# Kernel tuning notes

Hardware: AMD Instinct MI355X
Metric: run time of the kernel (lower is better)

Reference implementation:

```python
import jax, jax.numpy as jnp
import numpy as np

B, C, D, H, W = 2, 16, 64, 64, 64
HD, WD = 128, 128            # X-ray detector size
P = 3                        # offset_points
SPACING = (1.0, 1.0, 1.0)
SDR = 200.0
DEL = 2.0
BN_EPS = 1e-5


def _xray_coords(D, H, W, Hd, Wd, spacing, sdr, del_size):
    """Replicates _get_initial_xray geometry; pure constants -> numpy. Returns [D,H,W,2] float32."""
    theta, phi, gamma = np.pi, 0.0, np.pi / 2
    Rz = np.array([[np.cos(theta), -np.sin(theta), 0.0], [np.sin(theta), np.cos(theta), 0.0], [0.0, 0.0, 1.0]])
    Ry = np.array([[np.cos(phi), 0.0, np.sin(phi)], [0.0, 1.0, 0.0], [-np.sin(phi), 0.0, np.cos(phi)]])
    Rx = np.array([[1.0, 0.0, 0.0], [0.0, np.cos(gamma), -np.sin(gamma)], [0.0, np.sin(gamma), np.cos(gamma)]])
    R = sdr * (Rz @ Ry @ Rx)
    trans = np.array([D, H, W]) * np.array(spacing) / 2.0
    source = R[:, 0] + trans           # [3]
    center = -R[:, 0] + trans          # [3]
    Rn = R / np.linalg.norm(R, axis=-1, keepdims=True)   # row-normalize (torch normalize dim=-1)
    u, v = Rn[:, 1], Rn[:, 2]
    basis = np.stack([u, v])           # [2,3]
    h_off = 1.0 if Hd % 2 else 0.5
    w_off = 1.0 if Wd % 2 else 0.5
    t = (np.arange(-Hd // 2, Hd // 2) + h_off) * del_size
    s = (np.arange(-Wd // 2, Wd // 2) + w_off) * del_size
    coefs = np.stack(np.meshgrid(t, s, indexing='ij'), -1).reshape(-1, 2)   # cartesian_prod(t,s)
    target = coefs @ basis + center    # [Hd*Wd, 3]
    tz = np.arange(D) * spacing[2]
    tx = np.arange(H) * spacing[0]
    ty = np.arange(W) * spacing[1]
    pz, px_, py_ = np.meshgrid(tz, tx, ty, indexing='ij')
    p_n = np.stack([pz.ravel(), px_.ravel(), py_.ravel()], 1)   # [D*H*W, 3]
    wgt = (center[0] - source[0]) / (p_n[:, 0] - source[0])
    X = wgt[:, None] * (p_n - source) + source
    tmin = target.min(0)
    tmax = target.max(0)
    X = np.clip(X, tmin, tmax)
    delta = np.array([del_size, del_size]) @ basis              # [3]; component 0 is 0 and dropped
    Xc = (X[:, 1:] - tmin[1:]) / delta[1:]
    return Xc.reshape(D, H, W, 2).astype(np.float32)


def _conv3d(x, w, b):
    y = jax.lax.conv_general_dilated(x, w, (1, 1, 1), ((1, 1), (1, 1), (1, 1)),
                                     dimension_numbers=('NCDHW', 'OIDHW', 'NCDHW'))
    return y + b[None, :, None, None, None]


def _corner_weights(py, px, y0, y1, x0, x1):
    y0f, y1f = y0.astype(py.dtype), y1.astype(py.dtype)
    x0f, x1f = x0.astype(px.dtype), x1.astype(px.dtype)
    g_lt = (1 + (y0f - py)) * (1 + (x0f - px))
    g_rb = (1 - (y1f - py)) * (1 - (x1f - px))
    g_rt = (1 + (y0f - py)) * (1 - (x1f - px))
    g_lb = (1 - (y1f - py)) * (1 + (x0f - px))
    return g_lt, g_rb, g_rt, g_lb


def _corners(py, px, Ht, Wt):
    fy, fx = jnp.floor(py), jnp.floor(px)
    y0 = jnp.clip(fy, 0, Ht - 1).astype(jnp.int32)
    y1 = jnp.clip(fy + 1, 0, Ht - 1).astype(jnp.int32)
    x0 = jnp.clip(fx, 0, Wt - 1).astype(jnp.int32)
    x1 = jnp.clip(fx + 1, 0, Wt - 1).astype(jnp.int32)
    return y0, y1, x0, x1


def _bilerp_single(p, x):
    # p: [D,H,W,2] batch-independent coords; x: [B,C,Ht,Wt]
    Bx, Cx, Ht, Wt = x.shape
    py, px = p[..., 0], p[..., 1]
    y0, y1, x0, x1 = _corners(py, px, Ht, Wt)
    glt, grb, grt, glb = _corner_weights(py, px, y0, y1, x0, x1)
    xf = x.reshape(Bx, Cx, Ht * Wt)
    gat = lambda yy, xx: jnp.take(xf, yy * Wt + xx, axis=2)   # [B,C,D,H,W]
    return glt * gat(y0, x0) + grb * gat(y1, x1) + grt * gat(y0, x1) + glb * gat(y1, x0)


def _bilerp_multi(py, px, x):
    # py, px: [B,D,H,W,P]; x: [B,C,Ht,Wt] (padded X-ray)
    Bx, Cx, Ht, Wt = x.shape
    y0, y1, x0, x1 = _corners(py, px, Ht, Wt)
    glt, grb, grt, glb = _corner_weights(py, px, y0, y1, x0, x1)
    xf = x.reshape(Bx, Cx, Ht * Wt)

    def gat(yy, xx):
        idx = yy * Wt + xx                                    # [B,D,H,W,P]
        g = jax.vmap(lambda xb, ib: jnp.take(xb, ib, axis=1))(xf, idx.reshape(Bx, -1))
        return g.reshape(Bx, Cx, *idx.shape[1:])              # [B,C,D,H,W,P]

    e = lambda g: g[:, None]                                  # add channel dim
    return e(glt) * gat(y0, x0) + e(grb) * gat(y1, x1) + e(grt) * gat(y0, x1) + e(glb) * gat(y1, x0)


def _forward(CT, Xray, pW, pb, mW, mb, w1, b1, w2, b2, bn_gamma, bn_beta, bn_mean, bn_var):
    Bc, Cc, Dc, Hc, Wc = CT.shape
    Hd, Wd = Xray.shape[2], Xray.shape[3]
    Pp = mW.shape[0]
    Xrc = jnp.asarray(_xray_coords(Dc, Hc, Wc, Hd, Wd, SPACING, SDR, DEL))   # [D,H,W,2]
    xi = _bilerp_single(Xrc, Xray)                        # [B,C,D,H,W]
    CT_mix = jnp.concatenate([CT, xi], axis=1)            # [B,2C,D,H,W]
    Xp = jnp.pad(Xray, ((0, 0), (0, 0), (1, 1), (1, 1)))  # ZeroPad2d(1)
    offset = _conv3d(CT_mix, pW, pb)                      # [B,2P,D,H,W]
    m = jax.nn.softmax(_conv3d(CT_mix, mW, mb), axis=1)   # [B,P,D,H,W]
    oc = jnp.transpose(offset, (0, 2, 3, 4, 1))           # [B,D,H,W,2P]
    py = jnp.clip(oc[..., :Pp] + Xrc[..., :1] + 1.0, 0, Hd + 1)
    px = jnp.clip(oc[..., Pp:] + Xrc[..., 1:] + 1.0, 0, Wd + 1)
    p_coor = jnp.concatenate([py, px], axis=-1)
    Xoff = _bilerp_multi(py, px, Xp)                      # [B,C,D,H,W,P]
    mm = jnp.transpose(m, (0, 2, 3, 4, 1))[:, None]       # [B,1,D,H,W,P]
    Xsum = jnp.sum(Xoff * mm, axis=-1)                    # [B,C,D,H,W]
    h = _conv3d(jnp.concatenate([CT, Xsum], axis=1), w1, b1)
    sh = (1, -1, 1, 1, 1)
    h = (h - bn_mean.reshape(sh)) * jax.lax.rsqrt(bn_var.reshape(sh) + BN_EPS) * bn_gamma.reshape(sh) + bn_beta.reshape(sh)
    h = jnp.where(h >= 0, h, 0.2 * h)                     # LeakyReLU(0.2)
    return _conv3d(h, w2, b2), p_coor


def setup_inputs() -> dict:
    key = jax.random.key(0)
    ks = jax.random.split(key, 16)
    return {
        'CT': jax.random.normal(ks[0], (B, C, D, H, W), jnp.float32),
        'Xray': jax.random.normal(ks[1], (B, C, HD, WD), jnp.float32),
        'pW': jax.random.normal(ks[2], (2 * P, 2 * C, 3, 3, 3), jnp.float32) * 0.02,
        'pb': jax.random.normal(ks[3], (2 * P,), jnp.float32) * 0.01,
        'mW': jax.random.normal(ks[4], (P, 2 * C, 3, 3, 3), jnp.float32) * 0.02,
        'mb': jax.random.normal(ks[5], (P,), jnp.float32) * 0.01,
        'w1': jax.random.normal(ks[6], (C, 2 * C, 3, 3, 3), jnp.float32) * 0.02,
        'b1': jax.random.normal(ks[7], (C,), jnp.float32) * 0.01,
        'w2': jax.random.normal(ks[8], (C, C, 3, 3, 3), jnp.float32) * 0.02,
        'b2': jax.random.normal(ks[9], (C,), jnp.float32) * 0.01,
        'bn_gamma': 1.0 + 0.1 * jax.random.normal(ks[10], (C,), jnp.float32),
        'bn_beta': 0.1 * jax.random.normal(ks[11], (C,), jnp.float32),
        'bn_mean': 0.1 * jax.random.normal(ks[12], (C,), jnp.float32),
        'bn_var': jax.random.uniform(ks[13], (C,), jnp.float32, 0.5, 1.5),
    }


def reference(CT, Xray, pW, pb, mW, mb, w1, b1, w2, b2, bn_gamma, bn_beta, bn_mean, bn_var):
    return _forward(CT, Xray, pW, pb, mW, mb, w1, b1, w2, b2, bn_gamma, bn_beta, bn_mean, bn_var)
```

## Files before the change

### kernel.cpp

```cpp
#include <hip/hip_runtime.h>
#include <hip/hip_bf16.h>
#include <math.h>

constexpr int Dd = 64, Hh = 64, Ww = 64;
constexpr int HD = 128, WD = 128;
constexpr int DHW = Dd * Hh * Ww;
constexpr int HW = Hh * Ww;
constexpr int PD = 66;
constexpr int PS3 = PD * PD * PD;
constexpr int XT_S = 128 * 128;
constexpr int XP_S = 130 * 130;

using short8 = __attribute__((ext_vector_type(8))) short;
using f32x4  = __attribute__((ext_vector_type(4))) float;

struct Geom {
    double s0, s1, s2;
    double c0ms0;
    double tmin1, tmax1, tmin2, tmax2;
    double d1, d2;
};

__device__ __forceinline__ void xray_coord(const Geom g, int z, int x, int y,
                                           float& py, float& px) {
    double wgt = g.c0ms0 / ((double)z - g.s0);
    double X1 = wgt * ((double)x - g.s1) + g.s1;
    X1 = fmin(fmax(X1, g.tmin1), g.tmax1);
    double X2 = wgt * ((double)y - g.s2) + g.s2;
    X2 = fmin(fmax(X2, g.tmin2), g.tmax2);
    py = (float)((X1 - g.tmin1) / g.d1);
    px = (float)((X2 - g.tmin2) / g.d2);
}

__device__ __forceinline__ float bf2f(unsigned short u) {
    union { unsigned int i; float f; } v;
    v.i = ((unsigned int)u) << 16;
    return v.f;
}
__device__ __forceinline__ unsigned short f2bf(float f) {
    __hip_bfloat16 h = __float2bfloat16(f);
    return *reinterpret_cast<unsigned short*>(&h);
}

template <int CIN, int NK>
__global__ __launch_bounds__(256) void k_wprep(const float* __restrict__ w6,
                                               const float* __restrict__ w3,
                                               unsigned short* __restrict__ wB) {
    int i = blockIdx.x * 256 + threadIdx.x;
    if (i >= NK * 64 * 8) return;
    int s = i >> 9, l = (i >> 3) & 63, j = i & 7;
    int n = l & 15, q = l >> 4;
    int k = s * 32 + q * 8 + j;
    int tap = k / CIN, ci = k % CIN;
    float v = 0.f;
    if (tap < 27) {
        if (w3 == nullptr) {
            v = w6[(n * CIN + ci) * 27 + tap];
        } else {
            if (n < 6) v = w6[(n * CIN + ci) * 27 + tap];
            else if (n < 9) v = w3[((n - 6) * CIN + ci) * 27 + tap];
        }
    }
    wB[i] = f2bf(v);
}

__global__ void k_bias9(const float* __restrict__ pb, const float* __restrict__ mb,
                        float* __restrict__ b9) {
    int i = threadIdx.x;
    if (i < 16) b9[i] = (i < 6) ? pb[i] : ((i < 9) ? mb[i - 6] : 0.f);
}

__global__ __launch_bounds__(256) void k_xrayT(const float* __restrict__ X,
                                               unsigned short* __restrict__ XT) {
    int i = blockIdx.x * 256 + threadIdx.x;
    if (i >= 2 * XT_S) return;
    int b = i / XT_S, sp = i % XT_S;
    const float* src = X + (size_t)b * 16 * XT_S + sp;
    unsigned short* o = XT + (size_t)i * 16;
#pragma unroll
    for (int c = 0; c < 16; ++c) o[c] = f2bf(src[(size_t)c * XT_S]);
}

__global__ __launch_bounds__(256) void k_xpT(const float* __restrict__ X,
                                             unsigned short* __restrict__ XP) {
    int i = blockIdx.x * 256 + threadIdx.x;
    if (i >= 2 * XP_S) return;
    int b = i / XP_S, rc = i % XP_S;
    int r = rc / 130, c = rc % 130;
    unsigned short o[16];
    if (r >= 1 && r <= 128 && c >= 1 && c <= 128) {
        const float* src = X + (size_t)b * 16 * XT_S + (r - 1) * 128 + (c - 1);
#pragma unroll
        for (int ch = 0; ch < 16; ++ch) o[ch] = f2bf(src[(size_t)ch * XT_S]);
    } else {
#pragma unroll
        for (int ch = 0; ch < 16; ++ch) o[ch] = 0;
    }
    uint4* dst = (uint4*)(XP + (size_t)i * 16);
    uint4* s4 = (uint4*)o;
    dst[0] = s4[0]; dst[1] = s4[1];
}

__global__ __launch_bounds__(256) void k_prep_nin(const float* __restrict__ CT,
                                                  const unsigned short* __restrict__ XT,
                                                  unsigned short* __restrict__ nin,
                                                  Geom g) {
    int vox = blockIdx.x * 256 + threadIdx.x;
    int b = blockIdx.y;
    int z = vox >> 12, x = (vox >> 6) & 63, y = vox & 63;
    unsigned short outv[32];
    const float* ct = CT + (size_t)b * 16 * DHW + vox;
#pragma unroll
    for (int c = 0; c < 16; ++c) outv[c] = f2bf(ct[(size_t)c * DHW]);
    float py, px;
    xray_coord(g, z, x, y, py, px);
    float fy = floorf(py), fx = floorf(px);
    int y0 = (int)fminf(fmaxf(fy, 0.f), 127.f);
    int y1 = (int)fminf(fmaxf(fy + 1.f, 0.f), 127.f);
    int x0 = (int)fminf(fmaxf(fx, 0.f), 127.f);
    int x1 = (int)fminf(fmaxf(fx + 1.f, 0.f), 127.f);
    float y0f = (float)y0, y1f = (float)y1, x0f = (float)x0, x1f = (float)x1;
    float glt = (1.f + (y0f - py)) * (1.f + (x0f - px));
    float grb = (1.f - (y1f - py)) * (1.f - (x1f - px));
    float grt = (1.f + (y0f - py)) * (1.f - (x1f - px));
    float glb = (1.f - (y1f - py)) * (1.f + (x0f - px));
    const unsigned short* base = XT + (size_t)b * XT_S * 16;
    const unsigned short* p00 = base + (size_t)(y0 * 128 + x0) * 16;
    const unsigned short* p11 = base + (size_t)(y1 * 128 + x1) * 16;
    const unsigned short* p01 = base + (size_t)(y0 * 128 + x1) * 16;
    const unsigned short* p10 = base + (size_t)(y1 * 128 + x0) * 16;
#pragma unroll
    for (int c = 0; c < 16; ++c) {
        float v = glt * bf2f(p00[c]) + grb * bf2f(p11[c]) +
                  grt * bf2f(p01[c]) + glb * bf2f(p10[c]);
        outv[16 + c] = f2bf(v);
    }
    size_t pp = (((size_t)(z + 1)) * PD + (x + 1)) * PD + (y + 1);
    uint4* dst = (uint4*)(nin + ((size_t)b * PS3 + pp) * 32);
    uint4* s4 = (uint4*)outv;
    dst[0] = s4[0]; dst[1] = s4[1]; dst[2] = s4[2]; dst[3] = s4[3];
}

template <int CIN, int NK, int MODE>
__global__ __launch_bounds__(256) void k_conv_mfma(
    const unsigned short* __restrict__ IN, const unsigned short* __restrict__ wB,
    const float* __restrict__ bias,
    const float* __restrict__ bng, const float* __restrict__ bnb,
    const float* __restrict__ bnm, const float* __restrict__ bnv,
    float* __restrict__ outF, unsigned short* __restrict__ outH) {
    constexpr int NSLOT = CIN / 8;
    constexpr int SSH = (NSLOT == 4) ? 2 : 1;
    constexpr int NCHUNK = NSLOT * 648;
    __shared__ unsigned short lds[NSLOT * 648 * 8];

    int tid = threadIdx.x;
    int bid = blockIdx.x;
    int zt = bid & 15, xt = (bid >> 4) & 15, yt = bid >> 8;
    int b = blockIdx.y;

    const unsigned short* gsrc = IN + (size_t)b * PS3 * CIN;
    for (int d = tid; d < NCHUNK; d += 256) {
        int slot = d & (NSLOT - 1);
        int sp = d >> SSH;
        int zz = sp / 108;
        int rem = sp - zz * 108;
        int xx = rem / 18, yy = rem - xx * 18;
        size_t gp = (((size_t)(zt * 4 + zz)) * PD + (xt * 4 + xx)) * PD + (yt * 16 + yy);
        uint4 v = *(const uint4*)(gsrc + gp * CIN + slot * 8);
        *(uint4*)&lds[(size_t)(slot * 648 + sp) * 8] = v;
    }

    int lane = tid & 63;
    short8 bw[NK];
    {
        const short8* wsrc = (const short8*)wB;
#pragma unroll
        for (int s = 0; s < NK; ++s) bw[s] = wsrc[s * 64 + lane];
    }
    int col = lane & 15, q = lane >> 4;
    float bcol = bias[col];
    float bsc = 1.f, bsh = 0.f;
    if (MODE == 1) {
        float sc = bng[col] * rsqrtf(bnv[col] + 1e-5f);
        bsc = sc;
        bsh = bnb[col] - bnm[col] * sc;
    }
    __syncthreads();

    int w = tid >> 6;
    for (int vx = 0; vx < 4; ++vx) {
        f32x4 acc = {0.f, 0.f, 0.f, 0.f};
#pragma unroll
        for (int s = 0; s < NK; ++s) {
            int tap = (s * 32 + q * 8) / CIN;
            if (CIN == 16) tap = min(tap, 26);
            int slot = q & (NSLOT - 1);
            int dz = tap / 9;
            int trem = tap - dz * 9;
            int dx = trem / 3, dy = trem - dx * 3;
            int addr = ((slot * 648) + (w + dz) * 108 + (vx + dx) * 18 + col + dy) * 8;
            short8 a = *(const short8*)&lds[addr];
            acc = __builtin_amdgcn_mfma_f32_16x16x32_bf16(a, bw[s], acc, 0, 0, 0);
        }
        int z = zt * 4 + w, x = xt * 4 + vx;
        int yb = yt * 16 + q * 4;
        if (MODE == 0) {
            int vox = z * HW + x * 64 + yb;
            float* o = outF + ((size_t)b * DHW + vox) * 16 + col;
#pragma unroll
            for (int r = 0; r < 4; ++r) o[(size_t)r * 16] = acc[r] + bcol;
        } else if (MODE == 1) {
            size_t pp = (((size_t)(z + 1)) * PD + (x + 1)) * PD + (yb + 1);
            unsigned short* o = outH + ((size_t)b * PS3 + pp) * 16 + col;
#pragma unroll
            for (int r = 0; r < 4; ++r) {
                float v = acc[r] + bcol;
                v = v * bsc + bsh;
                v = (v >= 0.f) ? v : 0.2f * v;
                o[(size_t)r * 16] = f2bf(v);
            }
        } else {
            int vox = z * HW + x * 64 + yb;
            float* o = outF + ((size_t)b * 16 + col) * DHW + vox;
#pragma unroll
            for (int r = 0; r < 4; ++r) o[r] = acc[r] + bcol;
        }
    }
}

__global__ __launch_bounds__(256) void k_deform2(const float* __restrict__ offm,
                                                 const unsigned short* __restrict__ XP,
                                                 unsigned short* __restrict__ nin,
                                                 float* __restrict__ pcoor, Geom g) {
    int idx = blockIdx.x * 256 + threadIdx.x;
    int b = idx >> 18;
    int vox = idx & (DHW - 1);
    int z = vox >> 12, x = (vox >> 6) & 63, y = vox & 63;
    float bpy, bpx;
    xray_coord(g, z, x, y, bpy, bpx);
    const float* ob = offm + ((size_t)b * DHW + vox) * 16;
    float off[6];
#pragma unroll
    for (int k = 0; k < 6; ++k) off[k] = ob[k];
    float mv0 = ob[6], mv1 = ob[7], mv2 = ob[8];
    float mx = fmaxf(mv0, fmaxf(mv1, mv2));
    float e0 = __expf(mv0 - mx), e1 = __expf(mv1 - mx), e2 = __expf(mv2 - mx);
    float inv = 1.f / (e0 + e1 + e2);
    float ms[3] = {e0 * inv, e1 * inv, e2 * inv};

    float pys[3], pxs[3];
#pragma unroll
    for (int p = 0; p < 3; ++p) {
        pys[p] = fminf(fmaxf(off[p] + bpy + 1.f, 0.f), 129.f);
        pxs[p] = fminf(fmaxf(off[3 + p] + bpx + 1.f, 0.f), 129.f);
    }
    float* pc = pcoor + (size_t)idx * 6;
    pc[0] = pys[0]; pc[1] = pys[1]; pc[2] = pys[2];
    pc[3] = pxs[0]; pc[4] = pxs[1]; pc[5] = pxs[2];

    float acc[16];
#pragma unroll
    for (int c = 0; c < 16; ++c) acc[c] = 0.f;
    const unsigned short* xpb = XP + (size_t)b * XP_S * 16;
#pragma unroll
    for (int p = 0; p < 3; ++p) {
        float py = pys[p], px = pxs[p];
        float fy = floorf(py), fx = floorf(px);
        int y0 = (int)fminf(fmaxf(fy, 0.f), 129.f);
        int y1 = (int)fminf(fmaxf(fy + 1.f, 0.f), 129.f);
        int x0 = (int)fminf(fmaxf(fx, 0.f), 129.f);
        int x1 = (int)fminf(fmaxf(fx + 1.f, 0.f), 129.f);
        float y0f = (float)y0, y1f = (float)y1, x0f = (float)x0, x1f = (float)x1;
        float glt = (1.f + (y0f - py)) * (1.f + (x0f - px));
        float grb = (1.f - (y1f - py)) * (1.f - (x1f - px));
        float grt = (1.f + (y0f - py)) * (1.f - (x1f - px));
        float glb = (1.f - (y1f - py)) * (1.f + (x0f - px));
        const unsigned short* p00 = xpb + (size_t)(y0 * 130 + x0) * 16;
        const unsigned short* p11 = xpb + (size_t)(y1 * 130 + x1) * 16;
        const unsigned short* p01 = xpb + (size_t)(y0 * 130 + x1) * 16;
        const unsigned short* p10 = xpb + (size_t)(y1 * 130 + x0) * 16;
        float mp = ms[p];
#pragma unroll
        for (int c = 0; c < 16; ++c) {
            float v = glt * bf2f(p00[c]) + grb * bf2f(p11[c]) +
                      grt * bf2f(p01[c]) + glb * bf2f(p10[c]);
            acc[c] += mp * v;
        }
    }
    size_t pp = (((size_t)(z + 1)) * PD + (x + 1)) * PD + (y + 1);
    unsigned short outv[16];
#pragma unroll
    for (int c = 0; c < 16; ++c) outv[c] = f2bf(acc[c]);
    uint4* dst = (uint4*)(nin + ((size_t)b * PS3 + pp) * 32 + 16);
    uint4* s4 = (uint4*)outv;
    dst[0] = s4[0]; dst[1] = s4[1];
}

static void compute_geom(Geom& g) {
    const double sdr = 200.0, del = 2.0;
    double theta = M_PI, phi = 0.0, gam = M_PI / 2;
    double Rz[3][3] = {{cos(theta), -sin(theta), 0}, {sin(theta), cos(theta), 0}, {0, 0, 1}};
    double Ry[3][3] = {{cos(phi), 0, sin(phi)}, {0, 1, 0}, {-sin(phi), 0, cos(phi)}};
    double Rx[3][3] = {{1, 0, 0}, {0, cos(gam), -sin(gam)}, {0, sin(gam), cos(gam)}};
    double M[3][3], R[3][3];
    for (int i = 0; i < 3; i++)
        for (int j = 0; j < 3; j++) {
            double s = 0;
            for (int k = 0; k < 3; k++) s += Rz[i][k] * Ry[k][j];
            M[i][j] = s;
        }
    for (int i = 0; i < 3; i++)
        for (int j = 0; j < 3; j++) {
            double s = 0;
            for (int k = 0; k < 3; k++) s += M[i][k] * Rx[k][j];
            R[i][j] = sdr * s;
        }
    double trans[3] = {32.0, 32.0, 32.0};
    double src[3], ctr[3];
    for (int k = 0; k < 3; k++) {
        src[k] = R[k][0] + trans[k];
        ctr[k] = -R[k][0] + trans[k];
    }
    double Rn[3][3];
    for (int i = 0; i < 3; i++) {
        double n = sqrt(R[i][0] * R[i][0] + R[i][1] * R[i][1] + R[i][2] * R[i][2]);
        for (int j = 0; j < 3; j++) Rn[i][j] = R[i][j] / n;
    }
    double u[3], v[3];
    for (int k = 0; k < 3; k++) { u[k] = Rn[k][1]; v[k] = Rn[k][2]; }
    double tmin[3], tmax[3];
    for (int k = 0; k < 3; k++) {
        double a = 127.0 * fabs(u[k]) + 127.0 * fabs(v[k]);
        tmin[k] = ctr[k] - a;
        tmax[k] = ctr[k] + a;
    }
    double delta[3];
    for (int k = 0; k < 3; k++) delta[k] = del * u[k] + del * v[k];
    g.s0 = src[0]; g.s1 = src[1]; g.s2 = src[2];
    g.c0ms0 = ctr[0] - src[0];
    g.tmin1 = tmin[1]; g.tmax1 = tmax[1];
    g.tmin2 = tmin[2]; g.tmax2 = tmax[2];
    g.d1 = delta[1]; g.d2 = delta[2];
}

constexpr size_t NIN_B  = (size_t)2 * PS3 * 32 * 2;
constexpr size_t NH_B   = (size_t)2 * PS3 * 16 * 2;
constexpr size_t OFFM_B = (size_t)2 * DHW * 16 * 4;
constexpr size_t XT_B   = (size_t)2 * XT_S * 16 * 2;
constexpr size_t XP_B   = (size_t)2 * XP_S * 16 * 2;
constexpr size_t WB9_B  = (size_t)27 * 64 * 8 * 2;
constexpr size_t WB1_B  = WB9_B;
constexpr size_t WB2_B  = (size_t)14 * 64 * 8 * 2;

constexpr size_t O_NIN  = 0;
constexpr size_t O_NH   = O_NIN + NIN_B;
constexpr size_t O_OFFM = O_NH + NH_B;
constexpr size_t O_XT   = O_OFFM + OFFM_B;
constexpr size_t O_XP   = O_XT + XT_B;
constexpr size_t O_WB9  = O_XP + XP_B;
constexpr size_t O_WB1  = O_WB9 + WB9_B;
constexpr size_t O_WB2  = O_WB1 + WB1_B;
constexpr size_t O_B9   = O_WB2 + WB2_B;

extern "C" void kernel_launch(void* const* d_in, const int* in_sizes, int n_in,
                              void* d_out, int out_size, void* d_ws, size_t ws_size,
                              hipStream_t stream) {
    (void)in_sizes; (void)n_in; (void)out_size; (void)ws_size;
    const float* CT = (const float*)d_in[0];
    const float* Xray = (const float*)d_in[1];
    const float* pW = (const float*)d_in[2];
    const float* pb = (const float*)d_in[3];
    const float* mW = (const float*)d_in[4];
    const float* mb = (const float*)d_in[5];
    const float* w1 = (const float*)d_in[6];
    const float* b1 = (const float*)d_in[7];
    const float* w2 = (const float*)d_in[8];
    const float* b2 = (const float*)d_in[9];
    const float* bng = (const float*)d_in[10];
    const float* bnb = (const float*)d_in[11];
    const float* bnm = (const float*)d_in[12];
    const float* bnv = (const float*)d_in[13];

    char* ws = (char*)d_ws;
    unsigned short* nin = (unsigned short*)(ws + O_NIN);
    unsigned short* nh  = (unsigned short*)(ws + O_NH);
    float* offm = (float*)(ws + O_OFFM);
    unsigned short* XT = (unsigned short*)(ws + O_XT);
    unsigned short* XP = (unsigned short*)(ws + O_XP);
    unsigned short* wB9 = (unsigned short*)(ws + O_WB9);
    unsigned short* wB1 = (unsigned short*)(ws + O_WB1);
    unsigned short* wB2 = (unsigned short*)(ws + O_WB2);
    float* b9 = (float*)(ws + O_B9);

    float* out0 = (float*)d_out;
    float* out1 = out0 + (size_t)32 * DHW;

    Geom g;
    compute_geom(g);

    hipMemsetAsync(nin, 0, NIN_B, stream);
    hipMemsetAsync(nh, 0, NH_B, stream);

    k_wprep<32, 27><<<54, 256, 0, stream>>>(pW, mW, wB9);
    k_wprep<32, 27><<<54, 256, 0, stream>>>(w1, nullptr, wB1);
    k_wprep<16, 14><<<28, 256, 0, stream>>>(w2, nullptr, wB2);
    k_bias9<<<1, 64, 0, stream>>>(pb, mb, b9);

    k_xrayT<<<(2 * XT_S + 255) / 256, 256, 0, stream>>>(Xray, XT);
    k_xpT<<<(2 * XP_S + 255) / 256, 256, 0, stream>>>(Xray, XP);

    k_prep_nin<<<dim3(DHW / 256, 2), 256, 0, stream>>>(CT, XT, nin, g);

    k_conv_mfma<32, 27, 0><<<dim3(1024, 2), 256, 0, stream>>>(
        nin, wB9, b9, nullptr, nullptr, nullptr, nullptr, offm, nullptr);

    k_deform2<<<(2 * DHW) / 256, 256, 0, stream>>>(offm, XP, nin, out1, g);

    k_conv_mfma<32, 27, 1><<<dim3(1024, 2), 256, 0, stream>>>(
        nin, wB1, b1, bng, bnb, bnm, bnv, nullptr, nh);

    k_conv_mfma<16, 14, 2><<<dim3(1024, 2), 256, 0, stream>>>(
        nh, wB2, b2, nullptr, nullptr, nullptr, nullptr, out0, nullptr);
}
```

Before: 246.7 us.

## Fuse offset/mask conv with deformable sampling and drop padded buffers

Merges the offset/mask convolution with the deformable X-ray sampling into one kernel. The conv results are staged in shared memory instead of going to a global fp32 offm buffer and being read back by a separate kernel. Activations now use unpadded 64^3 layouts with bounds-checked halo loads, which removes both memsets of the padded buffers. The deformed features go to a separate xs buffer that the second conv reads as its upper channel slots. In exchange, every conv tile load pays extra boundary checks, and the fused kernel carries higher register and shared-memory pressure.

```diff
diff --git a/kernel.cpp b/kernel.cpp
--- a/kernel.cpp
+++ b/kernel.cpp
@@ -3,11 +3,8 @@
 #include <math.h>
 
 constexpr int Dd = 64, Hh = 64, Ww = 64;
-constexpr int HD = 128, WD = 128;
 constexpr int DHW = Dd * Hh * Ww;
 constexpr int HW = Hh * Ww;
-constexpr int PD = 66;
-constexpr int PS3 = PD * PD * PD;
 constexpr int XT_S = 128 * 128;
 constexpr int XP_S = 130 * 130;
 
@@ -135,66 +132,59 @@
                   grt * bf2f(p01[c]) + glb * bf2f(p10[c]);
         outv[16 + c] = f2bf(v);
     }
-    size_t pp = (((size_t)(z + 1)) * PD + (x + 1)) * PD + (y + 1);
-    uint4* dst = (uint4*)(nin + ((size_t)b * PS3 + pp) * 32);
+    uint4* dst = (uint4*)(nin + ((size_t)b * DHW + vox) * 32);
     uint4* s4 = (uint4*)outv;
     dst[0] = s4[0]; dst[1] = s4[1]; dst[2] = s4[2]; dst[3] = s4[3];
 }
 
-template <int CIN, int NK, int MODE>
-__global__ __launch_bounds__(256) void k_conv_mfma(
+__global__ __launch_bounds__(256) void k_conv9_deform(
     const unsigned short* __restrict__ IN, const unsigned short* __restrict__ wB,
-    const float* __restrict__ bias,
-    const float* __restrict__ bng, const float* __restrict__ bnb,
-    const float* __restrict__ bnm, const float* __restrict__ bnv,
-    float* __restrict__ outF, unsigned short* __restrict__ outH) {
-    constexpr int NSLOT = CIN / 8;
-    constexpr int SSH = (NSLOT == 4) ? 2 : 1;
-    constexpr int NCHUNK = NSLOT * 648;
-    __shared__ unsigned short lds[NSLOT * 648 * 8];
+    const float* __restrict__ bias, const unsigned short* __restrict__ XP,
+    unsigned short* __restrict__ xs, float* __restrict__ pcoor, Geom g) {
+    __shared__ char smem[4 * 648 * 8 * 2];
+    unsigned short* lds = (unsigned short*)smem;
+    float* ptile = (float*)smem;
 
     int tid = threadIdx.x;
     int bid = blockIdx.x;
     int zt = bid & 15, xt = (bid >> 4) & 15, yt = bid >> 8;
     int b = blockIdx.y;
 
-    const unsigned short* gsrc = IN + (size_t)b * PS3 * CIN;
-    for (int d = tid; d < NCHUNK; d += 256) {
-        int slot = d & (NSLOT - 1);
-        int sp = d >> SSH;
+    const unsigned short* gsrc = IN + (size_t)b * DHW * 32;
+    for (int d = tid; d < 4 * 648; d += 256) {
+        int slot = d & 3;
+        int sp = d >> 2;
         int zz = sp / 108;
         int rem = sp - zz * 108;
         int xx = rem / 18, yy = rem - xx * 18;
-        size_t gp = (((size_t)(zt * 4 + zz)) * PD + (xt * 4 + xx)) * PD + (yt * 16 + yy);
-        uint4 v = *(const uint4*)(gsrc + gp * CIN + slot * 8);
+        int gz = zt * 4 + zz - 1, gx = xt * 4 + xx - 1, gy = yt * 16 + yy - 1;
+        uint4 v = {0u, 0u, 0u, 0u};
+        if ((unsigned)gz < 64u && (unsigned)gx < 64u && (unsigned)gy < 64u) {
+            size_t gp = (size_t)gz * HW + gx * 64 + gy;
+            v = *(const uint4*)(gsrc + gp * 32 + slot * 8);
+        }
         *(uint4*)&lds[(size_t)(slot * 648 + sp) * 8] = v;
     }
 
     int lane = tid & 63;
-    short8 bw[NK];
+    short8 bw[27];
     {
         const short8* wsrc = (const short8*)wB;
 #pragma unroll
-        for (int s = 0; s < NK; ++s) bw[s] = wsrc[s * 64 + lane];
+        for (int s = 0; s < 27; ++s) bw[s] = wsrc[s * 64 + lane];
     }
     int col = lane & 15, q = lane >> 4;
     float bcol = bias[col];
-    float bsc = 1.f, bsh = 0.f;
-    if (MODE == 1) {
-        float sc = bng[col] * rsqrtf(bnv[col] + 1e-5f);
-        bsc = sc;
-        bsh = bnb[col] - bnm[col] * sc;
-    }
     __syncthreads();
 
     int w = tid >> 6;
+    float accs[4][4];
     for (int vx = 0; vx < 4; ++vx) {
         f32x4 acc = {0.f, 0.f, 0.f, 0.f};
 #pragma unroll
-        for (int s = 0; s < NK; ++s) {
-            int tap = (s * 32 + q * 8) / CIN;
-            if (CIN == 16) tap = min(tap, 26);
-            int slot = q & (NSLOT - 1);
+        for (int s = 0; s < 27; ++s) {
+            int tap = s;
+            int slot = q & 3;
             int dz = tap / 9;
             int trem = tap - dz * 9;
             int dx = trem / 3, dy = trem - dx * 3;
@@ -202,69 +192,50 @@
             short8 a = *(const short8*)&lds[addr];
             acc = __builtin_amdgcn_mfma_f32_16x16x32_bf16(a, bw[s], acc, 0, 0, 0);
         }
-        int z = zt * 4 + w, x = xt * 4 + vx;
-        int yb = yt * 16 + q * 4;
-        if (MODE == 0) {
-            int vox = z * HW + x * 64 + yb;
-            float* o = outF + ((size_t)b * DHW + vox) * 16 + col;
-#pragma unroll
-            for (int r = 0; r < 4; ++r) o[(size_t)r * 16] = acc[r] + bcol;
-        } else if (MODE == 1) {
-            size_t pp = (((size_t)(z + 1)) * PD + (x + 1)) * PD + (yb + 1);
-            unsigned short* o = outH + ((size_t)b * PS3 + pp) * 16 + col;
-#pragma unroll
-            for (int r = 0; r < 4; ++r) {
-                float v = acc[r] + bcol;
-                v = v * bsc + bsh;
-                v = (v >= 0.f) ? v : 0.2f * v;
-                o[(size_t)r * 16] = f2bf(v);
-            }
-        } else {
-            int vox = z * HW + x * 64 + yb;
-            float* o = outF + ((size_t)b * 16 + col) * DHW + vox;
-#pragma unroll
-            for (int r = 0; r < 4; ++r) o[r] = acc[r] + bcol;
-        }
-    }
-}
-
-__global__ __launch_bounds__(256) void k_deform2(const float* __restrict__ offm,
-                                                 const unsigned short* __restrict__ XP,
-                                                 unsigned short* __restrict__ nin,
-                                                 float* __restrict__ pcoor, Geom g) {
-    int idx = blockIdx.x * 256 + threadIdx.x;
-    int b = idx >> 18;
-    int vox = idx & (DHW - 1);
-    int z = vox >> 12, x = (vox >> 6) & 63, y = vox & 63;
+#pragma unroll
+        for (int r = 0; r < 4; ++r) accs[vx][r] = acc[r] + bcol;
+    }
+    __syncthreads();
+#pragma unroll
+    for (int vx = 0; vx < 4; ++vx)
+#pragma unroll
+        for (int r = 0; r < 4; ++r)
+            ptile[(w * 64 + vx * 16 + q * 4 + r) * 17 + col] = accs[vx][r];
+    __syncthreads();
+
+    int z = zt * 4 + (tid >> 6);
+    int x = xt * 4 + ((tid >> 4) & 3);
+    int y = yt * 16 + (tid & 15);
+    int vox = z * HW + x * 64 + y;
+    const float* pt = &ptile[tid * 17];
     float bpy, bpx;
     xray_coord(g, z, x, y, bpy, bpx);
-    const float* ob = offm + ((size_t)b * DHW + vox) * 16;
-    float off[6];
-#pragma unroll
-    for (int k = 0; k < 6; ++k) off[k] = ob[k];
-    float mv0 = ob[6], mv1 = ob[7], mv2 = ob[8];
+    float off0 = pt[0], off1 = pt[1], off2 = pt[2];
+    float off3 = pt[3], off4 = pt[4], off5 = pt[5];
+    float mv0 = pt[6], mv1 = pt[7], mv2 = pt[8];
     float mx = fmaxf(mv0, fmaxf(mv1, mv2));
     float e0 = __expf(mv0 - mx), e1 = __expf(mv1 - mx), e2 = __expf(mv2 - mx);
     float inv = 1.f / (e0 + e1 + e2);
     float ms[3] = {e0 * inv, e1 * inv, e2 * inv};
 
-    float pys[3], pxs[3];
+    float pys[3], pxs3[3];
+    pys[0] = fminf(fmaxf(off0 + bpy + 1.f, 0.f), 129.f);
+    pys[1] = fminf(fmaxf(off1 + bpy + 1.f, 0.f), 129.f);
+    pys[2] = fminf(fmaxf(off2 + bpy + 1.f, 0.f), 129.f);
+    pxs3[0] = fminf(fmaxf(off3 + bpx + 1.f, 0.f), 129.f);
+    pxs3[1] = fminf(fmaxf(off4 + bpx + 1.f, 0.f), 129.f);
+    pxs3[2] = fminf(fmaxf(off5 + bpx + 1.f, 0.f), 129.f);
+    float* pc = pcoor + ((size_t)b * DHW + vox) * 6;
+    pc[0] = pys[0]; pc[1] = pys[1]; pc[2] = pys[2];
+    pc[3] = pxs3[0]; pc[4] = pxs3[1]; pc[5] = pxs3[2];
+
+    float acc16[16];
+#pragma unroll
+    for (int c = 0; c < 16; ++c) acc16[c] = 0.f;
+    const unsigned short* xpb = XP + (size_t)b * XP_S * 16;
 #pragma unroll
     for (int p = 0; p < 3; ++p) {
-        pys[p] = fminf(fmaxf(off[p] + bpy + 1.f, 0.f), 129.f);
-        pxs[p] = fminf(fmaxf(off[3 + p] + bpx + 1.f, 0.f), 129.f);
-    }
-    float* pc = pcoor + (size_t)idx * 6;
-    pc[0] = pys[0]; pc[1] = pys[1]; pc[2] = pys[2];
-    pc[3] = pxs[0]; pc[4] = pxs[1]; pc[5] = pxs[2];
-
-    float acc[16];
-#pragma unroll
-    for (int c = 0; c < 16; ++c) acc[c] = 0.f;
-    const unsigned short* xpb = XP + (size_t)b * XP_S * 16;
-#pragma unroll
-    for (int p = 0; p < 3; ++p) {
-        float py = pys[p], px = pxs[p];
+        float py = pys[p], px = pxs3[p];
         float fy = floorf(py), fx = floorf(px);
         int y0 = (int)fminf(fmaxf(fy, 0.f), 129.f);
         int y1 = (int)fminf(fmaxf(fy + 1.f, 0.f), 129.f);
@@ -284,16 +255,107 @@
         for (int c = 0; c < 16; ++c) {
             float v = glt * bf2f(p00[c]) + grb * bf2f(p11[c]) +
                       grt * bf2f(p01[c]) + glb * bf2f(p10[c]);
-            acc[c] += mp * v;
-        }
-    }
-    size_t pp = (((size_t)(z + 1)) * PD + (x + 1)) * PD + (y + 1);
+            acc16[c] += mp * v;
+        }
+    }
     unsigned short outv[16];
 #pragma unroll
-    for (int c = 0; c < 16; ++c) outv[c] = f2bf(acc[c]);
-    uint4* dst = (uint4*)(nin + ((size_t)b * PS3 + pp) * 32 + 16);
+    for (int c = 0; c < 16; ++c) outv[c] = f2bf(acc16[c]);
+    uint4* dst = (uint4*)(xs + ((size_t)b * DHW + vox) * 16);
     uint4* s4 = (uint4*)outv;
     dst[0] = s4[0]; dst[1] = s4[1];
+}
+
+template <int CIN, int NK, int MODE>
+__global__ __launch_bounds__(256) void k_conv_mfma(
+    const unsigned short* __restrict__ IN, const unsigned short* __restrict__ IN2,
+    const unsigned short* __restrict__ wB, const float* __restrict__ bias,
+    const float* __restrict__ bng, const float* __restrict__ bnb,
+    const float* __restrict__ bnm, const float* __restrict__ bnv,
+    float* __restrict__ outF, unsigned short* __restrict__ outH) {
+    constexpr int NSLOT = CIN / 8;
+    constexpr int SSH = (NSLOT == 4) ? 2 : 1;
+    constexpr int NCHUNK = NSLOT * 648;
+    __shared__ unsigned short lds[NSLOT * 648 * 8];
+
+    int tid = threadIdx.x;
+    int bid = blockIdx.x;
+    int zt = bid & 15, xt = (bid >> 4) & 15, yt = bid >> 8;
+    int b = blockIdx.y;
+
+    const unsigned short* src1 = IN + (size_t)b * DHW * ((MODE == 1) ? 32 : 16);
+    const unsigned short* src2 =
+        (MODE == 1) ? (IN2 + (size_t)b * DHW * 16) : nullptr;
+    for (int d = tid; d < NCHUNK; d += 256) {
+        int slot = d & (NSLOT - 1);
+        int sp = d >> SSH;
+        int zz = sp / 108;
+        int rem = sp - zz * 108;
+        int xx = rem / 18, yy = rem - xx * 18;
+        int gz = zt * 4 + zz - 1, gx = xt * 4 + xx - 1, gy = yt * 16 + yy - 1;
+        uint4 v = {0u, 0u, 0u, 0u};
+        if ((unsigned)gz < 64u && (unsigned)gx < 64u && (unsigned)gy < 64u) {
+            size_t gp = (size_t)gz * HW + gx * 64 + gy;
+            if (MODE == 1) {
+                if (slot < 2) v = *(const uint4*)(src1 + gp * 32 + slot * 8);
+                else v = *(const uint4*)(src2 + gp * 16 + (slot - 2) * 8);
+            } else {
+                v = *(const uint4*)(src1 + gp * 16 + slot * 8);
+            }
+        }
+        *(uint4*)&lds[(size_t)(slot * 648 + sp) * 8] = v;
+    }
+
+    int lane = tid & 63;
+    short8 bw[NK];
+    {
+        const short8* wsrc = (const short8*)wB;
+#pragma unroll
+        for (int s = 0; s < NK; ++s) bw[s] = wsrc[s * 64 + lane];
+    }
+    int col = lane & 15, q = lane >> 4;
+    float bcol = bias[col];
+    float bsc = 1.f, bsh = 0.f;
+    if (MODE == 1) {
+        float sc = bng[col] * rsqrtf(bnv[col] + 1e-5f);
+        bsc = sc;
+        bsh = bnb[col] - bnm[col] * sc;
+    }
+    __syncthreads();
+
+    int w = tid >> 6;
+    for (int vx = 0; vx < 4; ++vx) {
+        f32x4 acc = {0.f, 0.f, 0.f, 0.f};
+#pragma unroll
+        for (int s = 0; s < NK; ++s) {
+            int tap = (s * 32 + q * 8) / CIN;
+            if (CIN == 16) tap = min(tap, 26);
+            int slot = q & (NSLOT - 1);
+            int dz = tap / 9;
+            int trem = tap - dz * 9;
+            int dx = trem / 3, dy = trem - dx * 3;
+            int addr = ((slot * 648) + (w + dz) * 108 + (vx + dx) * 18 + col + dy) * 8;
+            short8 a = *(const short8*)&lds[addr];
+            acc = __builtin_amdgcn_mfma_f32_16x16x32_bf16(a, bw[s], acc, 0, 0, 0);
+        }
+        int z = zt * 4 + w, x = xt * 4 + vx;
+        int yb = yt * 16 + q * 4;
+        int vox = z * HW + x * 64 + yb;
+        if (MODE == 1) {
+            unsigned short* o = outH + ((size_t)b * DHW + vox) * 16 + col;
+#pragma unroll
+            for (int r = 0; r < 4; ++r) {
+                float v = acc[r] + bcol;
+                v = v * bsc + bsh;
+                v = (v >= 0.f) ? v : 0.2f * v;
+                o[(size_t)r * 16] = f2bf(v);
+            }
+        } else {
+            float* o = outF + ((size_t)b * 16 + col) * DHW + vox;
+#pragma unroll
+            for (int r = 0; r < 4; ++r) o[r] = acc[r] + bcol;
+        }
+    }
 }
 
 static void compute_geom(Geom& g) {
@@ -343,24 +405,24 @@
     g.d1 = delta[1]; g.d2 = delta[2];
 }
 
-constexpr size_t NIN_B  = (size_t)2 * PS3 * 32 * 2;
-constexpr size_t NH_B   = (size_t)2 * PS3 * 16 * 2;
-constexpr size_t OFFM_B = (size_t)2 * DHW * 16 * 4;
-constexpr size_t XT_B   = (size_t)2 * XT_S * 16 * 2;
-constexpr size_t XP_B   = (size_t)2 * XP_S * 16 * 2;
-constexpr size_t WB9_B  = (size_t)27 * 64 * 8 * 2;
-constexpr size_t WB1_B  = WB9_B;
-constexpr size_t WB2_B  = (size_t)14 * 64 * 8 * 2;
-
-constexpr size_t O_NIN  = 0;
-constexpr size_t O_NH   = O_NIN + NIN_B;
-constexpr size_t O_OFFM = O_NH + NH_B;
-constexpr size_t O_XT   = O_OFFM + OFFM_B;
-constexpr size_t O_XP   = O_XT + XT_B;
-constexpr size_t O_WB9  = O_XP + XP_B;
-constexpr size_t O_WB1  = O_WB9 + WB9_B;
-constexpr size_t O_WB2  = O_WB1 + WB1_B;
-constexpr size_t O_B9   = O_WB2 + WB2_B;
+constexpr size_t NIN_B = (size_t)2 * DHW * 32 * 2;
+constexpr size_t XS_B  = (size_t)2 * DHW * 16 * 2;
+constexpr size_t NH_B  = XS_B;
+constexpr size_t XT_B  = (size_t)2 * XT_S * 16 * 2;
+constexpr size_t XP_B  = (size_t)2 * XP_S * 16 * 2;
+constexpr size_t WB9_B = (size_t)27 * 64 * 8 * 2;
+constexpr size_t WB1_B = WB9_B;
+constexpr size_t WB2_B = (size_t)14 * 64 * 8 * 2;
+
+constexpr size_t O_NIN = 0;
+constexpr size_t O_XS  = O_NIN + NIN_B;
+constexpr size_t O_NH  = O_XS + XS_B;
+constexpr size_t O_XT  = O_NH + NH_B;
+constexpr size_t O_XP  = O_XT + XT_B;
+constexpr size_t O_WB9 = O_XP + XP_B;
+constexpr size_t O_WB1 = O_WB9 + WB9_B;
+constexpr size_t O_WB2 = O_WB1 + WB1_B;
+constexpr size_t O_B9  = O_WB2 + WB2_B;
 
 extern "C" void kernel_launch(void* const* d_in, const int* in_sizes, int n_in,
                               void* d_out, int out_size, void* d_ws, size_t ws_size,
@@ -383,10 +445,10 @@
 
     char* ws = (char*)d_ws;
     unsigned short* nin = (unsigned short*)(ws + O_NIN);
+    unsigned short* xs  = (unsigned short*)(ws + O_XS);
     unsigned short* nh  = (unsigned short*)(ws + O_NH);
-    float* offm = (float*)(ws + O_OFFM);
-    unsigned short* XT = (unsigned short*)(ws + O_XT);
-    unsigned short* XP = (unsigned short*)(ws + O_XP);
+    unsigned short* XT  = (unsigned short*)(ws + O_XT);
+    unsigned short* XP  = (unsigned short*)(ws + O_XP);
     unsigned short* wB9 = (unsigned short*)(ws + O_WB9);
     unsigned short* wB1 = (unsigned short*)(ws + O_WB1);
     unsigned short* wB2 = (unsigned short*)(ws + O_WB2);
@@ -398,9 +460,6 @@
     Geom g;
     compute_geom(g);
 
-    hipMemsetAsync(nin, 0, NIN_B, stream);
-    hipMemsetAsync(nh, 0, NH_B, stream);
-
     k_wprep<32, 27><<<54, 256, 0, stream>>>(pW, mW, wB9);
     k_wprep<32, 27><<<54, 256, 0, stream>>>(w1, nullptr, wB1);
     k_wprep<16, 14><<<28, 256, 0, stream>>>(w2, nullptr, wB2);
@@ -411,14 +470,11 @@
 
     k_prep_nin<<<dim3(DHW / 256, 2), 256, 0, stream>>>(CT, XT, nin, g);
 
-    k_conv_mfma<32, 27, 0><<<dim3(1024, 2), 256, 0, stream>>>(
-        nin, wB9, b9, nullptr, nullptr, nullptr, nullptr, offm, nullptr);
-
-    k_deform2<<<(2 * DHW) / 256, 256, 0, stream>>>(offm, XP, nin, out1, g);
+    k_conv9_deform<<<dim3(1024, 2), 256, 0, stream>>>(nin, wB9, b9, XP, xs, out1, g);
 
     k_conv_mfma<32, 27, 1><<<dim3(1024, 2), 256, 0, stream>>>(
-        nin, wB1, b1, bng, bnb, bnm, bnv, nullptr, nh);
+        nin, xs, wB1, b1, bng, bnb, bnm, bnv, nullptr, nh);
 
     k_conv_mfma<16, 14, 2><<<dim3(1024, 2), 256, 0, stream>>>(
-        nh, wB2, b2, nullptr, nullptr, nullptr, nullptr, out0, nullptr);
-}
+        nh, nullptr, wB2, b2, nullptr, nullptr, nullptr, nullptr, out0, nullptr);
+}
```

Measured after the change: 225.1 us. -8.8%, faster.
